# Performance work log

Hardware: AMD Instinct MI355X
Metric: run time of the kernel (lower is better)

The kernel has to match this reference:

```python
import jax, jax.numpy as jnp
import numpy as np

BATCH, SEQ, EMBED, HIDDEN, VOCAB = 32, 64, 512, 512, 32000

def setup_inputs() -> dict:
    key = jax.random.key(0)
    ks = jax.random.split(key, 11)
    s = lambda k, shape, scale: jax.random.normal(k, shape, dtype=jnp.float32) * scale
    return {
        "features": s(ks[0], (BATCH, HIDDEN), 1.0),
        "captions": jax.random.randint(ks[1], (BATCH, SEQ), 0, VOCAB),
        "embedding": s(ks[2], (VOCAB, EMBED), 1.0),
        "Wz_w": s(ks[3], (HIDDEN, EMBED + HIDDEN), 0.03),
        "Wz_b": s(ks[4], (HIDDEN,), 0.03),
        "Wr_w": s(ks[5], (HIDDEN, EMBED + HIDDEN), 0.03),
        "Wr_b": s(ks[6], (HIDDEN,), 0.03),
        "Wh_w": s(ks[7], (HIDDEN, EMBED + HIDDEN), 0.03),
        "Wh_b": s(ks[8], (HIDDEN,), 0.03),
        "fc_w": s(ks[9], (VOCAB, HIDDEN), 0.03),
        "fc_b": s(ks[10], (VOCAB,), 0.03),
    }

def reference(features, captions, embedding, Wz_w, Wz_b, Wr_w, Wr_b, Wh_w, Wh_b, fc_w, fc_b):
    # embeddings: [B, T, E] -> scan over time with xs [T, B, E]
    emb = embedding[captions]                      # [B, T, E]
    xs = jnp.swapaxes(emb, 0, 1)                   # [T, B, E]

    def step(h, x_t):
        comb = jnp.concatenate([x_t, h], axis=1)                   # [B, E+H]
        z = jax.nn.sigmoid(comb @ Wz_w.T + Wz_b)                   # update gate
        r = jax.nn.sigmoid(comb @ Wr_w.T + Wr_b)                   # reset gate
        comb_r = jnp.concatenate([x_t, r * h], axis=1)
        h_tilde = jnp.tanh(comb_r @ Wh_w.T + Wh_b)
        h_new = (1.0 - z) * h + z * h_tilde
        return h_new, h_new

    _, hs = jax.lax.scan(step, features, xs)       # hs: [T, B, H]
    hs = jnp.swapaxes(hs, 0, 1)                    # [B, T, H]
    # output projection done once over all timesteps (same math as per-step fc_out)
    logits = jnp.einsum('bth,vh->btv', hs, fc_w) + fc_b  # [B, T, V]
    return logits
```

## Files before the change

kernel.cpp:

```cpp
#include <hip/hip_runtime.h>
#include <hip/hip_bf16.h>

typedef __bf16 bf16;
typedef __bf16 bf16x8 __attribute__((ext_vector_type(8)));
typedef float f32x4 __attribute__((ext_vector_type(4)));
typedef unsigned int u32x4 __attribute__((ext_vector_type(4)));

#define B_SZ 32
#define T_SZ 64
#define H_SZ 512
#define V_SZ 32000
#define NWG_REC 8
#define NTILES 250
#define MTILES 16

__device__ __forceinline__ float sigmoidf_(float v) { return 1.0f / (1.0f + expf(-v)); }

__device__ __forceinline__ bf16x8 cvt8(const float* __restrict__ p) {
  float4 a = *(const float4*)p;
  float4 b = *(const float4*)(p + 4);
  bf16x8 o;
  o[0] = (bf16)a.x; o[1] = (bf16)a.y; o[2] = (bf16)a.z; o[3] = (bf16)a.w;
  o[4] = (bf16)b.x; o[5] = (bf16)b.y; o[6] = (bf16)b.z; o[7] = (bf16)b.w;
  return o;
}

#define GLD(dst, base, off) \
  asm volatile("global_load_dwordx4 %0, %1, off offset:" off " sc0 sc1" \
               : "=v"(dst) : "v"(base))
#define LOADALL(af, base) do { \
  GLD(af[0],  base, "0");   GLD(af[1],  base, "64");  GLD(af[2],  base, "128"); GLD(af[3],  base, "192"); \
  GLD(af[4],  base, "256"); GLD(af[5],  base, "320"); GLD(af[6],  base, "384"); GLD(af[7],  base, "448"); \
  GLD(af[8],  base, "512"); GLD(af[9],  base, "576"); GLD(af[10], base, "640"); GLD(af[11], base, "704"); \
  GLD(af[12], base, "768"); GLD(af[13], base, "832"); GLD(af[14], base, "896"); GLD(af[15], base, "960"); \
} while (0)
#define GST2(base, off, val) do { \
  unsigned int w_ = (unsigned int)__builtin_bit_cast(unsigned short, (bf16)(val)); \
  asm volatile("global_store_short %0, %1, off offset:" off " sc0 sc1" \
               :: "v"(base), "v"(w_) : "memory"); \
} while (0)
#define WAITV  asm volatile("s_waitcnt vmcnt(0)" ::: "memory")
#define SCHEDB __builtin_amdgcn_sched_barrier(0)

__device__ __forceinline__ int llc_poll(const int* p) {
  int r;
  asm volatile("global_load_dword %0, %1, off sc0 sc1\n\ts_waitcnt vmcnt(0)"
               : "=v"(r) : "v"(p) : "memory");
  return r;
}

__global__ __launch_bounds__(256) void xproj_k(
    const int* __restrict__ caps, const float* __restrict__ emb,
    const float* __restrict__ B0, const float* __restrict__ B1, const float* __restrict__ B2,
    const float* __restrict__ bias0, const float* __restrict__ bias1, const float* __restrict__ bias2,
    float* __restrict__ C, int gemm_blocks, int prep_start,
    const float* __restrict__ fcw_src, bf16* __restrict__ fcw_dst,
    const float* __restrict__ feat, bf16* __restrict__ h_g, int* __restrict__ ctr,
    bf16* __restrict__ whp_dst)
{
  __shared__ __align__(16) bf16 lA[128 * 32];
  __shared__ __align__(16) bf16 lB[128 * 32];
  const int tid = threadIdx.x;
  const int bidx = blockIdx.x;

  if (bidx >= prep_start) {
    int i = (bidx - prep_start) * 256 + tid;
    int w = i >> 15;
    int rem = i & 32767;
    int n = rem >> 6;
    int k8 = (rem & 63) * 8;
    const float* W = (w == 0) ? B0 : (w == 1) ? B1 : B2;
    *(bf16x8*)(whp_dst + (long)w * 262144 + n * 512 + k8) = cvt8(W + (long)n * 1024 + 512 + k8);
    if (i < B_SZ * H_SZ) h_g[i] = (bf16)feat[i];
    if (i < 128) ctr[i] = 0;
    return;
  }

  if (bidx >= gemm_blocks) {
    long base = ((long)(bidx - gemm_blocks) * 256 + tid) * 8;
    const long stride = (long)128 * 256 * 8;
    for (long i = base; i < (long)V_SZ * H_SZ; i += stride)
      *(bf16x8*)(fcw_dst + i) = cvt8(fcw_src + i);
    return;
  }

  const int lane = tid & 63;
  const int l15  = lane & 15;
  const int kb8  = (lane >> 4) * 8;
  const int wid  = tid >> 6;
  const int wm   = wid >> 1, wn = wid & 1;
  const int mtile = bidx % 16, ntile = bidx / 16;
  const int m0 = mtile * 128, n0 = ntile * 128;

  int wsel = n0 >> 9;
  const float* Bv   = wsel == 0 ? B0 : wsel == 1 ? B1 : B2;
  const float* bias = wsel == 0 ? bias0 : wsel == 1 ? bias1 : bias2;
  int nb = n0 & 511;

  f32x4 acc[4][4] = {};

  for (int k0 = 0; k0 < 512; k0 += 32) {
    #pragma unroll
    for (int j = 0; j < 2; ++j) {
      int c = j * 256 + tid;
      int row = c >> 2;
      int kc = (c & 3) * 8;
      *(bf16x8*)&lA[row * 32 + kc] = cvt8(emb + (long)caps[m0 + row] * 512 + k0 + kc);
      *(bf16x8*)&lB[row * 32 + kc] = cvt8(Bv + (long)(nb + row) * 1024 + k0 + kc);
    }
    __syncthreads();
    bf16x8 af[4], bfr[4];
    #pragma unroll
    for (int mf = 0; mf < 4; ++mf)
      af[mf] = *(const bf16x8*)&lA[(wm * 64 + mf * 16 + l15) * 32 + kb8];
    #pragma unroll
    for (int nf = 0; nf < 4; ++nf)
      bfr[nf] = *(const bf16x8*)&lB[(wn * 64 + nf * 16 + l15) * 32 + kb8];
    #pragma unroll
    for (int mf = 0; mf < 4; ++mf)
      #pragma unroll
      for (int nf = 0; nf < 4; ++nf)
        acc[mf][nf] = __builtin_amdgcn_mfma_f32_16x16x32_bf16(af[mf], bfr[nf], acc[mf][nf], 0, 0, 0);
    __syncthreads();
  }

  #pragma unroll
  for (int mf = 0; mf < 4; ++mf)
    #pragma unroll
    for (int nf = 0; nf < 4; ++nf)
      #pragma unroll
      for (int r = 0; r < 4; ++r) {
        int row = m0 + wm * 64 + mf * 16 + (lane >> 4) * 4 + r;
        int lc  = wn * 64 + nf * 16 + l15;
        C[(long)row * 1536 + n0 + lc] = acc[mf][nf][r] + bias[nb + lc];
      }
}

__global__ __launch_bounds__(512, 1) void fused_k(
    const float* __restrict__ X,
    const bf16* __restrict__ Wzh, const bf16* __restrict__ Wrh, const bf16* __restrict__ Whh,
    const float* __restrict__ feat,
    bf16* __restrict__ h_g, bf16* __restrict__ rh_g,
    bf16* __restrict__ hs, int* __restrict__ ctr,
    const bf16* __restrict__ fcw16, const float* __restrict__ fcw_f32,
    const float* __restrict__ fc_b, float* __restrict__ out, int use_bf16B)
{
  __shared__ __align__(16) char smem[20480];
  const int tid  = threadIdx.x;
  const int bid  = blockIdx.x;
  const int lane = tid & 63;
  const int l15  = lane & 15;
  int* prog = ctr + 64;

  if (bid < NWG_REC) {
    char* ldsb = smem;
    const int u    = bid * 8 + (tid >> 6);
    const int kb   = (lane >> 4) * 8;
    const int rq   = (lane >> 4) * 4;
    const int b0   = (u >> 5) * 16;
    const int gcol = (u & 31) * 16 + l15;

    u32x4 Bz[16], Br[16];
    LOADALL(Bz, Wzh + (long)gcol * 512 + kb);
    LOADALL(Br, Wrh + (long)gcol * 512 + kb);
    WAITV;
    const bf16* whb = Whh + (long)gcol * 512 + kb;

    float hprev[4];
    #pragma unroll
    for (int r = 0; r < 4; ++r) hprev[r] = feat[(b0 + rq + r) * 512 + gcol];

    const float* xb = X + (long)(b0 + rq) * 64 * 1536 + gcol;
    float xz[4], xr[4];
    #pragma unroll
    for (int r = 0; r < 4; ++r) {
      xz[r] = xb[r * 98304];
      xr[r] = xb[r * 98304 + 512];
    }

    const int srow0 = tid >> 6;
    const int soff0 = (tid * 16) ^ ((srow0 & 7) << 4);
    const int soff1 = (8192 + tid * 16) ^ ((srow0 & 7) << 4);
    const int fbase = (l15 * 1024 + (lane >> 4) * 16) ^ ((l15 & 7) << 4);

    bf16* rhst = rh_g + (b0 + rq) * 512 + gcol;
    bf16* hst  = h_g  + (b0 + rq) * 512 + gcol;

    int epoch = 0;
    for (int t = 0; t < T_SZ; ++t) {
      {
        const bf16* src = h_g + b0 * 512;
        u32x4 v0, v1;
        GLD(v0, src + tid * 8, "0");
        GLD(v1, src + 4096 + tid * 8, "0");
        WAITV;
        SCHEDB;
        *(u32x4*)(ldsb + soff0) = v0;
        *(u32x4*)(ldsb + soff1) = v1;
      }
      __syncthreads();
      f32x4 ze = {}, re = {};
      #pragma unroll
      for (int kk = 0; kk < 16; ++kk) {
        bf16x8 a = *(const bf16x8*)(ldsb + (fbase ^ (kk * 64)));
        ze = __builtin_amdgcn_mfma_f32_16x16x32_bf16(a, __builtin_bit_cast(bf16x8, Bz[kk]), ze, 0, 0, 0);
        re = __builtin_amdgcn_mfma_f32_16x16x32_bf16(a, __builtin_bit_cast(bf16x8, Br[kk]), re, 0, 0, 0);
      }
      float xh[4];
      #pragma unroll
      for (int r = 0; r < 4; ++r) xh[r] = xb[r * 98304 + t * 1536 + 1024];
      f32x4 zf;
      {
        float r0 = sigmoidf_(re[0] + xr[0]) * hprev[0];
        float r1 = sigmoidf_(re[1] + xr[1]) * hprev[1];
        float r2 = sigmoidf_(re[2] + xr[2]) * hprev[2];
        float r3 = sigmoidf_(re[3] + xr[3]) * hprev[3];
        GST2(rhst, "0", r0); GST2(rhst, "1024", r1); GST2(rhst, "2048", r2); GST2(rhst, "3072", r3);
        #pragma unroll
        for (int r = 0; r < 4; ++r) zf[r] = sigmoidf_(ze[r] + xz[r]);
      }
      ++epoch;
      WAITV;
      __syncthreads();
      if (tid == 0) {
        __hip_atomic_fetch_add(ctr, 1, __ATOMIC_RELAXED, __HIP_MEMORY_SCOPE_AGENT);
        while (__hip_atomic_load(ctr, __ATOMIC_RELAXED, __HIP_MEMORY_SCOPE_AGENT) < NWG_REC * epoch)
          __builtin_amdgcn_s_sleep(1);
      }
      __syncthreads();

      {
        const bf16* src = rh_g + b0 * 512;
        u32x4 v0, v1;
        GLD(v0, src + tid * 8, "0");
        GLD(v1, src + 4096 + tid * 8, "0");
        WAITV;
        SCHEDB;
        *(u32x4*)(ldsb + soff0) = v0;
        *(u32x4*)(ldsb + soff1) = v1;
      }
      __syncthreads();
      f32x4 he = {};
      #pragma unroll
      for (int kk = 0; kk < 16; ++kk) {
        bf16x8 a = *(const bf16x8*)(ldsb + (fbase ^ (kk * 64)));
        u32x4 bh = *(const u32x4*)(whb + kk * 32);
        he = __builtin_amdgcn_mfma_f32_16x16x32_bf16(a, __builtin_bit_cast(bf16x8, bh), he, 0, 0, 0);
      }
      if (t + 1 < T_SZ) {
        #pragma unroll
        for (int r = 0; r < 4; ++r) {
          xz[r] = xb[r * 98304 + (t + 1) * 1536];
          xr[r] = xb[r * 98304 + (t + 1) * 1536 + 512];
        }
      }
      bf16* ph = hs + (long)(t * 32 + b0 + rq) * 512 + gcol;
      #pragma unroll
      for (int r = 0; r < 4; ++r) {
        float ht = tanhf(he[r] + xh[r]);
        float hn = hprev[r] + zf[r] * (ht - hprev[r]);
        hprev[r] = hn;
      }
      GST2(hst, "0", hprev[0]); GST2(hst, "1024", hprev[1]);
      GST2(hst, "2048", hprev[2]); GST2(hst, "3072", hprev[3]);
      GST2(ph, "0", hprev[0]); GST2(ph, "1024", hprev[1]);
      GST2(ph, "2048", hprev[2]); GST2(ph, "3072", hprev[3]);
      ++epoch;
      WAITV;
      __syncthreads();
      if (tid == 0) {
        __hip_atomic_fetch_add(ctr, 1, __ATOMIC_RELAXED, __HIP_MEMORY_SCOPE_AGENT);
        while (__hip_atomic_load(ctr, __ATOMIC_RELAXED, __HIP_MEMORY_SCOPE_AGENT) < NWG_REC * epoch)
          __builtin_amdgcn_s_sleep(1);
        if (bid == 0) {
          int e = epoch;
          asm volatile("global_store_dword %0, %1, off sc0 sc1" :: "v"(prog), "v"(e) : "memory");
        }
      }
      __syncthreads();
    }
    return;
  }

  const int lwg   = bid - NWG_REC;
  const int mtile = lwg / NTILES;
  const int ntile = lwg % NTILES;
  const int m0 = mtile * 128, n0 = ntile * 128;

  if (tid == 0) {
    const int tgt = 8 * (mtile + 1);
    while (llc_poll(prog) < tgt) __builtin_amdgcn_s_sleep(32);
  }
  __syncthreads();

  bf16* lA = (bf16*)smem;
  bf16* lB = (bf16*)(smem + 10240);
  const int kb8  = (lane >> 4) * 8;
  const int wid  = tid >> 6;
  const int wm   = wid >> 1;
  const int wn   = wid & 1;
  const int arow = tid >> 2;
  const int akc  = (tid & 3) * 8;

  f32x4 acc[2][4] = {};

  for (int k0 = 0; k0 < 512; k0 += 32) {
    u32x4 av;
    GLD(av, hs + (long)(m0 + arow) * 512 + k0 + akc, "0");
    bf16x8 bv;
    if (use_bf16B) bv = *(const bf16x8*)(fcw16 + (long)(n0 + arow) * 512 + k0 + akc);
    else           bv = cvt8(fcw_f32 + (long)(n0 + arow) * 512 + k0 + akc);
    WAITV;
    SCHEDB;
    *(u32x4*)&lA[arow * 40 + akc] = av;
    *(bf16x8*)&lB[arow * 40 + akc] = bv;
    __syncthreads();
    bf16x8 af[2], bfr[4];
    #pragma unroll
    for (int mf = 0; mf < 2; ++mf)
      af[mf] = *(const bf16x8*)&lA[(wm * 32 + mf * 16 + l15) * 40 + kb8];
    #pragma unroll
    for (int nf = 0; nf < 4; ++nf)
      bfr[nf] = *(const bf16x8*)&lB[(wn * 64 + nf * 16 + l15) * 40 + kb8];
    #pragma unroll
    for (int mf = 0; mf < 2; ++mf)
      #pragma unroll
      for (int nf = 0; nf < 4; ++nf)
        acc[mf][nf] = __builtin_amdgcn_mfma_f32_16x16x32_bf16(af[mf], bfr[nf], acc[mf][nf], 0, 0, 0);
    __syncthreads();
  }

  #pragma unroll
  for (int mf = 0; mf < 2; ++mf)
    #pragma unroll
    for (int nf = 0; nf < 4; ++nf) {
      int col = n0 + wn * 64 + nf * 16 + l15;
      float bias_v = fc_b[col];
      #pragma unroll
      for (int r = 0; r < 4; ++r) {
        int rr = m0 + wm * 32 + mf * 16 + (lane >> 4) * 4 + r;
        int tt = rr >> 5, b = rr & 31;
        out[(long)(b * 64 + tt) * 32000 + col] = acc[mf][nf][r] + bias_v;
      }
    }
}

extern "C" void kernel_launch(void* const* d_in, const int* in_sizes, int n_in,
                              void* d_out, int out_size, void* d_ws, size_t ws_size,
                              hipStream_t stream) {
  const float* feat = (const float*)d_in[0];
  const int*   caps = (const int*)d_in[1];
  const float* emb  = (const float*)d_in[2];
  const float* Wz_w = (const float*)d_in[3];
  const float* Wz_b = (const float*)d_in[4];
  const float* Wr_w = (const float*)d_in[5];
  const float* Wr_b = (const float*)d_in[6];
  const float* Wh_w = (const float*)d_in[7];
  const float* Wh_b = (const float*)d_in[8];
  const float* fc_w = (const float*)d_in[9];
  const float* fc_b = (const float*)d_in[10];
  float* out = (float*)d_out;

  char* ws = (char*)d_ws;
  float* X_all = (float*)(ws + 0);
  bf16*  h_g   = (bf16*) (ws + 12582912);
  bf16*  rh_g  = (bf16*) (ws + 12615680);
  bf16*  hs    = (bf16*) (ws + 12648448);
  bf16*  Whp   = (bf16*) (ws + 14745600);
  int*   ctr   = (int*)  (ws + 16318464);
  bf16*  fcw16 = (bf16*) (ws + 16318976);
  const bool cvt_fc = (ws_size >= (size_t)49087000);

  const int prep_start = cvt_fc ? 320 : 192;
  xproj_k<<<dim3(prep_start + 384), dim3(256), 0, stream>>>(
      caps, emb, Wz_w, Wr_w, Wh_w, Wz_b, Wr_b, Wh_b, X_all, 192, prep_start,
      fc_w, fcw16, feat, h_g, ctr, Whp);

  fused_k<<<dim3(NWG_REC + MTILES * NTILES), dim3(512), 0, stream>>>(
      X_all, Whp, Whp + 262144, Whp + 524288, feat, h_g, rh_g, hs, ctr,
      fcw16, fc_w, fc_b, out, cvt_fc ? 1 : 0);
}
```

Baseline: 646.8 us.

## Make FC workers persistent per vocab slice with LDS-resident weights

Replaces the 4000 per-tile FC workgroups with 500 persistent workers. Each worker converts its 64-row slice of fc_w to bf16 once, keeps it in LDS, then loops over the 16 M-tiles as the recurrence publishes them, loading A directly into registers. This drops the separate fc_w bf16 conversion pass and lets the weight load overlap the recurrence. The recurrence also moves its barrier-arrive atomics earlier so the sigmoid, x loads and next-step prefetch overlap the spin-wait. The cost is 64KB LDS per workgroup and occupancy bounds of 2, which may limit concurrency.

```diff
diff --git a/kernel.cpp b/kernel.cpp
--- a/kernel.cpp
+++ b/kernel.cpp
@@ -11,7 +11,7 @@
 #define H_SZ 512
 #define V_SZ 32000
 #define NWG_REC 8
-#define NTILES 250
+#define NWRK 500
 #define MTILES 16
 
 __device__ __forceinline__ float sigmoidf_(float v) { return 1.0f / (1.0f + expf(-v)); }
@@ -53,8 +53,7 @@
     const int* __restrict__ caps, const float* __restrict__ emb,
     const float* __restrict__ B0, const float* __restrict__ B1, const float* __restrict__ B2,
     const float* __restrict__ bias0, const float* __restrict__ bias1, const float* __restrict__ bias2,
-    float* __restrict__ C, int gemm_blocks, int prep_start,
-    const float* __restrict__ fcw_src, bf16* __restrict__ fcw_dst,
+    float* __restrict__ C, int prep_start,
     const float* __restrict__ feat, bf16* __restrict__ h_g, int* __restrict__ ctr,
     bf16* __restrict__ whp_dst)
 {
@@ -76,14 +75,6 @@
     return;
   }
 
-  if (bidx >= gemm_blocks) {
-    long base = ((long)(bidx - gemm_blocks) * 256 + tid) * 8;
-    const long stride = (long)128 * 256 * 8;
-    for (long i = base; i < (long)V_SZ * H_SZ; i += stride)
-      *(bf16x8*)(fcw_dst + i) = cvt8(fcw_src + i);
-    return;
-  }
-
   const int lane = tid & 63;
   const int l15  = lane & 15;
   const int kb8  = (lane >> 4) * 8;
@@ -136,27 +127,27 @@
       }
 }
 
-__global__ __launch_bounds__(512, 1) void fused_k(
+__global__ __launch_bounds__(512, 2) void fused_k(
     const float* __restrict__ X,
     const bf16* __restrict__ Wzh, const bf16* __restrict__ Wrh, const bf16* __restrict__ Whh,
     const float* __restrict__ feat,
     bf16* __restrict__ h_g, bf16* __restrict__ rh_g,
     bf16* __restrict__ hs, int* __restrict__ ctr,
-    const bf16* __restrict__ fcw16, const float* __restrict__ fcw_f32,
-    const float* __restrict__ fc_b, float* __restrict__ out, int use_bf16B)
+    const float* __restrict__ fcw, const float* __restrict__ fc_b, float* __restrict__ out)
 {
-  __shared__ __align__(16) char smem[20480];
+  __shared__ __align__(16) char smem[65536];
   const int tid  = threadIdx.x;
   const int bid  = blockIdx.x;
   const int lane = tid & 63;
   const int l15  = lane & 15;
+  const int q    = lane >> 4;
   int* prog = ctr + 64;
 
   if (bid < NWG_REC) {
     char* ldsb = smem;
     const int u    = bid * 8 + (tid >> 6);
-    const int kb   = (lane >> 4) * 8;
-    const int rq   = (lane >> 4) * 4;
+    const int kb   = q * 8;
+    const int rq   = q * 4;
     const int b0   = (u >> 5) * 16;
     const int gcol = (u & 31) * 16 + l15;
 
@@ -181,7 +172,7 @@
     const int srow0 = tid >> 6;
     const int soff0 = (tid * 16) ^ ((srow0 & 7) << 4);
     const int soff1 = (8192 + tid * 16) ^ ((srow0 & 7) << 4);
-    const int fbase = (l15 * 1024 + (lane >> 4) * 16) ^ ((l15 & 7) << 4);
+    const int fbase = (l15 * 1024 + q * 16) ^ ((l15 & 7) << 4);
 
     bf16* rhst = rh_g + (b0 + rq) * 512 + gcol;
     bf16* hst  = h_g  + (b0 + rq) * 512 + gcol;
@@ -206,24 +197,25 @@
         ze = __builtin_amdgcn_mfma_f32_16x16x32_bf16(a, __builtin_bit_cast(bf16x8, Bz[kk]), ze, 0, 0, 0);
         re = __builtin_amdgcn_mfma_f32_16x16x32_bf16(a, __builtin_bit_cast(bf16x8, Br[kk]), re, 0, 0, 0);
       }
-      float xh[4];
-      #pragma unroll
-      for (int r = 0; r < 4; ++r) xh[r] = xb[r * 98304 + t * 1536 + 1024];
-      f32x4 zf;
       {
         float r0 = sigmoidf_(re[0] + xr[0]) * hprev[0];
         float r1 = sigmoidf_(re[1] + xr[1]) * hprev[1];
         float r2 = sigmoidf_(re[2] + xr[2]) * hprev[2];
         float r3 = sigmoidf_(re[3] + xr[3]) * hprev[3];
         GST2(rhst, "0", r0); GST2(rhst, "1024", r1); GST2(rhst, "2048", r2); GST2(rhst, "3072", r3);
-        #pragma unroll
-        for (int r = 0; r < 4; ++r) zf[r] = sigmoidf_(ze[r] + xz[r]);
       }
       ++epoch;
       WAITV;
       __syncthreads();
+      if (tid == 0)
+        __hip_atomic_fetch_add(ctr, 1, __ATOMIC_RELAXED, __HIP_MEMORY_SCOPE_AGENT);
+      f32x4 zf;
+      #pragma unroll
+      for (int r = 0; r < 4; ++r) zf[r] = sigmoidf_(ze[r] + xz[r]);
+      float xh[4];
+      #pragma unroll
+      for (int r = 0; r < 4; ++r) xh[r] = xb[r * 98304 + t * 1536 + 1024];
       if (tid == 0) {
-        __hip_atomic_fetch_add(ctr, 1, __ATOMIC_RELAXED, __HIP_MEMORY_SCOPE_AGENT);
         while (__hip_atomic_load(ctr, __ATOMIC_RELAXED, __HIP_MEMORY_SCOPE_AGENT) < NWG_REC * epoch)
           __builtin_amdgcn_s_sleep(1);
       }
@@ -247,6 +239,22 @@
         u32x4 bh = *(const u32x4*)(whb + kk * 32);
         he = __builtin_amdgcn_mfma_f32_16x16x32_bf16(a, __builtin_bit_cast(bf16x8, bh), he, 0, 0, 0);
       }
+      bf16* ph = hs + (long)(t * 32 + b0 + rq) * 512 + gcol;
+      #pragma unroll
+      for (int r = 0; r < 4; ++r) {
+        float ht = tanhf(he[r] + xh[r]);
+        float hn = hprev[r] + zf[r] * (ht - hprev[r]);
+        hprev[r] = hn;
+      }
+      GST2(hst, "0", hprev[0]); GST2(hst, "1024", hprev[1]);
+      GST2(hst, "2048", hprev[2]); GST2(hst, "3072", hprev[3]);
+      GST2(ph, "0", hprev[0]); GST2(ph, "1024", hprev[1]);
+      GST2(ph, "2048", hprev[2]); GST2(ph, "3072", hprev[3]);
+      ++epoch;
+      WAITV;
+      __syncthreads();
+      if (tid == 0)
+        __hip_atomic_fetch_add(ctr, 1, __ATOMIC_RELAXED, __HIP_MEMORY_SCOPE_AGENT);
       if (t + 1 < T_SZ) {
         #pragma unroll
         for (int r = 0; r < 4; ++r) {
@@ -254,22 +262,7 @@
           xr[r] = xb[r * 98304 + (t + 1) * 1536 + 512];
         }
       }
-      bf16* ph = hs + (long)(t * 32 + b0 + rq) * 512 + gcol;
-      #pragma unroll
-      for (int r = 0; r < 4; ++r) {
-        float ht = tanhf(he[r] + xh[r]);
-        float hn = hprev[r] + zf[r] * (ht - hprev[r]);
-        hprev[r] = hn;
-      }
-      GST2(hst, "0", hprev[0]); GST2(hst, "1024", hprev[1]);
-      GST2(hst, "2048", hprev[2]); GST2(hst, "3072", hprev[3]);
-      GST2(ph, "0", hprev[0]); GST2(ph, "1024", hprev[1]);
-      GST2(ph, "2048", hprev[2]); GST2(ph, "3072", hprev[3]);
-      ++epoch;
-      WAITV;
-      __syncthreads();
       if (tid == 0) {
-        __hip_atomic_fetch_add(ctr, 1, __ATOMIC_RELAXED, __HIP_MEMORY_SCOPE_AGENT);
         while (__hip_atomic_load(ctr, __ATOMIC_RELAXED, __HIP_MEMORY_SCOPE_AGENT) < NWG_REC * epoch)
           __builtin_amdgcn_s_sleep(1);
         if (bid == 0) {
@@ -282,67 +275,62 @@
     return;
   }
 
-  const int lwg   = bid - NWG_REC;
-  const int mtile = lwg / NTILES;
-  const int ntile = lwg % NTILES;
-  const int m0 = mtile * 128, n0 = ntile * 128;
-
-  if (tid == 0) {
-    const int tgt = 8 * (mtile + 1);
-    while (llc_poll(prog) < tgt) __builtin_amdgcn_s_sleep(32);
+  const int n0 = (bid - NWG_REC) * 64;
+  bf16* lB = (bf16*)smem;
+
+  #pragma unroll
+  for (int i = 0; i < 8; ++i) {
+    int c = i * 512 + tid;
+    int L = c * 16;
+    int j = L >> 10;
+    int k0 = (L & 1023) >> 1;
+    bf16x8 v = cvt8(fcw + (long)(n0 + j) * 512 + k0);
+    *(bf16x8*)((char*)lB + (L ^ ((j & 7) << 4))) = v;
   }
   __syncthreads();
 
-  bf16* lA = (bf16*)smem;
-  bf16* lB = (bf16*)(smem + 10240);
-  const int kb8  = (lane >> 4) * 8;
-  const int wid  = tid >> 6;
-  const int wm   = wid >> 1;
-  const int wn   = wid & 1;
-  const int arow = tid >> 2;
-  const int akc  = (tid & 3) * 8;
-
-  f32x4 acc[2][4] = {};
-
-  for (int k0 = 0; k0 < 512; k0 += 32) {
-    u32x4 av;
-    GLD(av, hs + (long)(m0 + arow) * 512 + k0 + akc, "0");
-    bf16x8 bv;
-    if (use_bf16B) bv = *(const bf16x8*)(fcw16 + (long)(n0 + arow) * 512 + k0 + akc);
-    else           bv = cvt8(fcw_f32 + (long)(n0 + arow) * 512 + k0 + akc);
+  const int wid = tid >> 6;
+  const int kb  = q * 8;
+  int fbB[4];
+  #pragma unroll
+  for (int nf = 0; nf < 4; ++nf) {
+    int j = nf * 16 + l15;
+    fbB[nf] = ((j << 10) + q * 16) ^ ((l15 & 7) << 4);
+  }
+  float bias_v[4];
+  #pragma unroll
+  for (int nf = 0; nf < 4; ++nf) bias_v[nf] = fc_b[n0 + nf * 16 + l15];
+
+  for (int m = 0; m < MTILES; ++m) {
+    if (tid == 0) {
+      const int tgt = 8 * (m + 1);
+      while (llc_poll(prog) < tgt) __builtin_amdgcn_s_sleep(32);
+    }
+    __syncthreads();
+
+    u32x4 af[16];
+    LOADALL(af, hs + (long)(m * 128 + wid * 16 + l15) * 512 + kb);
     WAITV;
     SCHEDB;
-    *(u32x4*)&lA[arow * 40 + akc] = av;
-    *(bf16x8*)&lB[arow * 40 + akc] = bv;
-    __syncthreads();
-    bf16x8 af[2], bfr[4];
-    #pragma unroll
-    for (int mf = 0; mf < 2; ++mf)
-      af[mf] = *(const bf16x8*)&lA[(wm * 32 + mf * 16 + l15) * 40 + kb8];
+    f32x4 acc[4] = {};
+    #pragma unroll
+    for (int kk = 0; kk < 16; ++kk) {
+      bf16x8 a = __builtin_bit_cast(bf16x8, af[kk]);
+      #pragma unroll
+      for (int nf = 0; nf < 4; ++nf) {
+        bf16x8 b = *(const bf16x8*)((char*)lB + (fbB[nf] ^ (kk * 64)));
+        acc[nf] = __builtin_amdgcn_mfma_f32_16x16x32_bf16(a, b, acc[nf], 0, 0, 0);
+      }
+    }
     #pragma unroll
     for (int nf = 0; nf < 4; ++nf)
-      bfr[nf] = *(const bf16x8*)&lB[(wn * 64 + nf * 16 + l15) * 40 + kb8];
-    #pragma unroll
-    for (int mf = 0; mf < 2; ++mf)
-      #pragma unroll
-      for (int nf = 0; nf < 4; ++nf)
-        acc[mf][nf] = __builtin_amdgcn_mfma_f32_16x16x32_bf16(af[mf], bfr[nf], acc[mf][nf], 0, 0, 0);
-    __syncthreads();
-  }
-
-  #pragma unroll
-  for (int mf = 0; mf < 2; ++mf)
-    #pragma unroll
-    for (int nf = 0; nf < 4; ++nf) {
-      int col = n0 + wn * 64 + nf * 16 + l15;
-      float bias_v = fc_b[col];
       #pragma unroll
       for (int r = 0; r < 4; ++r) {
-        int rr = m0 + wm * 32 + mf * 16 + (lane >> 4) * 4 + r;
+        int rr = m * 128 + wid * 16 + q * 4 + r;
         int tt = rr >> 5, b = rr & 31;
-        out[(long)(b * 64 + tt) * 32000 + col] = acc[mf][nf][r] + bias_v;
-      }
-    }
+        out[(long)(b * 64 + tt) * 32000 + n0 + nf * 16 + l15] = acc[nf][r] + bias_v[nf];
+      }
+  }
 }
 
 extern "C" void kernel_launch(void* const* d_in, const int* in_sizes, int n_in,
@@ -368,15 +356,12 @@
   bf16*  hs    = (bf16*) (ws + 12648448);
   bf16*  Whp   = (bf16*) (ws + 14745600);
   int*   ctr   = (int*)  (ws + 16318464);
-  bf16*  fcw16 = (bf16*) (ws + 16318976);
-  const bool cvt_fc = (ws_size >= (size_t)49087000);
-
-  const int prep_start = cvt_fc ? 320 : 192;
-  xproj_k<<<dim3(prep_start + 384), dim3(256), 0, stream>>>(
-      caps, emb, Wz_w, Wr_w, Wh_w, Wz_b, Wr_b, Wh_b, X_all, 192, prep_start,
-      fc_w, fcw16, feat, h_g, ctr, Whp);
-
-  fused_k<<<dim3(NWG_REC + MTILES * NTILES), dim3(512), 0, stream>>>(
+
+  xproj_k<<<dim3(576), dim3(256), 0, stream>>>(
+      caps, emb, Wz_w, Wr_w, Wh_w, Wz_b, Wr_b, Wh_b, X_all, 192,
+      feat, h_g, ctr, Whp);
+
+  fused_k<<<dim3(NWG_REC + NWRK), dim3(512), 0, stream>>>(
       X_all, Whp, Whp + 262144, Whp + 524288, feat, h_g, rh_g, hs, ctr,
-      fcw16, fc_w, fc_b, out, cvt_fc ? 1 : 0);
-}
+      fc_w, fc_b, out);
+}
```

Result: slower. 690.2 us (+6.7%).
